# Kernel tuning notes

Hardware: AMD Instinct MI355X
Metric: run time of the kernel (lower is better)

## Reference

```python
import jax, jax.numpy as jnp
import numpy as np

DIM = 768
N_HEAD = 12
HEAD_DIM = 64
INNER = N_HEAD * HEAD_DIM
SCALE = HEAD_DIM ** -0.5


def setup_inputs() -> dict:
    key = jax.random.key(0)
    ks = jax.random.split(key, 12)
    B, Sf, St = 4, 2048, 2048
    from_tensor = jax.random.normal(ks[0], (B, Sf, DIM), dtype=jnp.float32)
    to_tensor = jax.random.normal(ks[1], (B, St, DIM), dtype=jnp.float32)
    attention_mask = jax.random.randint(ks[2], (B, Sf, St), 0, 2, dtype=jnp.int32)
    # Dense layers: kernel ~ RandomNormal (stddev 0.05, keras default), bias zeros
    def kern(k, fan_in, fan_out):
        return 0.05 * jax.random.normal(k, (fan_in, fan_out), dtype=jnp.float32)
    return {
        "from_tensor": from_tensor,
        "to_tensor": to_tensor,
        "attention_mask": attention_mask,
        "Wq": kern(ks[3], DIM, INNER), "bq": jnp.zeros((INNER,), jnp.float32),
        "Wk": kern(ks[4], DIM, INNER), "bk": jnp.zeros((INNER,), jnp.float32),
        "Wv": kern(ks[5], DIM, INNER), "bv": jnp.zeros((INNER,), jnp.float32),
        "Wo": kern(ks[6], INNER, DIM), "bo": jnp.zeros((DIM,), jnp.float32),
    }


def reference(from_tensor, to_tensor, attention_mask, Wq, bq, Wk, bk, Wv, bv, Wo, bo):
    B, Sf, _ = from_tensor.shape
    St = to_tensor.shape[1]
    # projections -> [B, S, n_head, head_dim] -> [B, n_head, S, head_dim]
    def split_heads(x, S):
        return x.reshape(B, S, N_HEAD, HEAD_DIM).transpose(0, 2, 1, 3)
    q = split_heads(from_tensor @ Wq + bq, Sf) * SCALE
    k = split_heads(to_tensor @ Wk + bk, St)
    v = split_heads(to_tensor @ Wv + bv, St)
    # scores [B, H, Sf, St]
    scores = jnp.einsum('bhik,bhjk->bhij', q, k)
    adder = (1.0 - attention_mask.astype(jnp.float32)) * -10000.0
    scores = scores + adder[:, None, :, :]
    probs = jax.nn.softmax(scores, axis=-1)
    out = jnp.einsum('bhij,bhjk->bhik', probs, v)  # [B, H, Sf, Dh]
    out = out.transpose(0, 2, 1, 3).reshape(B, Sf, INNER)
    return out @ Wo + bo
```

## Files before the change

### kernel.cpp

```cpp
#include <hip/hip_runtime.h>
#include <stdint.h>

#define DIM 768
#define NH 12
#define HD 64
#define BSZ 4
#define SEQ 2048
#define MROWS (BSZ*SEQ)

typedef __attribute__((ext_vector_type(8))) short v8s;
typedef __attribute__((ext_vector_type(4))) float v4f;
typedef __attribute__((ext_vector_type(8))) _Float16 v8h;
typedef __attribute__((ext_vector_type(2))) __fp16 v2fp;

__device__ __forceinline__ uint16_t f2bf(float x) {
  union { float f; uint32_t u; } v; v.f = x;
  uint32_t r = v.u + 0x7fffu + ((v.u >> 16) & 1u);
  return (uint16_t)(r >> 16);
}

#if __has_builtin(__builtin_amdgcn_cvt_pk_bf16_f32)
typedef __attribute__((ext_vector_type(2))) __bf16 v2bf;
__device__ __forceinline__ uint32_t pack_bf16(float a, float b) {
  union { v2bf v; uint32_t u; } c;
  c.v = __builtin_amdgcn_cvt_pk_bf16_f32(a, b);
  return c.u;
}
#else
__device__ __forceinline__ uint32_t pack_bf16(float a, float b) {
  return (uint32_t)f2bf(a) | ((uint32_t)f2bf(b) << 16);
}
#endif

__device__ __forceinline__ uint32_t pack_f16(float a, float b) {
#if __has_builtin(__builtin_amdgcn_cvt_pkrtz)
  union { v2fp h; uint32_t u; } c;
  c.h = __builtin_amdgcn_cvt_pkrtz(a, b);
  return c.u;
#else
  union { _Float16 h[2]; uint32_t u; } c;
  c.h[0] = (_Float16)a; c.h[1] = (_Float16)b; return c.u;
#endif
}

__device__ __forceinline__ float fexp2(float x) {
#if __has_builtin(__builtin_amdgcn_exp2f)
  return __builtin_amdgcn_exp2f(x);
#else
  return exp2f(x);
#endif
}

__device__ __forceinline__ int sbfe1(uint32_t w, int off) {
#if __has_builtin(__builtin_amdgcn_sbfe)
  return __builtin_amdgcn_sbfe((int)w, off, 1);
#else
  return ((int)(w << (31 - off))) >> 31;
#endif
}
__device__ __forceinline__ float maskf(float x, int mext) {
  union { float f; int i; } u; u.f = x; u.i &= mext; return u.f;
}

__device__ __forceinline__ void gl16(const void* g, void* l) {
  __builtin_amdgcn_global_load_lds(
      (const __attribute__((address_space(1))) unsigned int*)g,
      (__attribute__((address_space(3))) unsigned int*)l, 16, 0, 0);
}

__global__ void cvt_bf16_kernel(const float* __restrict__ src0, uint16_t* __restrict__ dst0,
                                const float* __restrict__ src1, uint16_t* __restrict__ dst1,
                                int n4) {
  int i = blockIdx.x * blockDim.x + threadIdx.x;
  const float* src = (i < n4) ? src0 : src1;
  uint16_t* dst = (i < n4) ? dst0 : dst1;
  int j = (i < n4) ? i : i - n4;
  float4 v = ((const float4*)src)[j];
  ushort4 o;
  o.x = f2bf(v.x); o.y = f2bf(v.y); o.z = f2bf(v.z); o.w = f2bf(v.w);
  ((ushort4*)dst)[j] = o;
}

__global__ void mask_bits_kernel(const int* __restrict__ src,
                                 unsigned long long* __restrict__ dst, int nwords) {
  int gtid = blockIdx.x * blockDim.x + threadIdx.x;
  int w = gtid >> 6;
  int lane = threadIdx.x & 63;
  if (w >= nwords) return;
  int b  = w >> 16;
  int q  = (w >> 5) & 2047;
  int kt = w & 31;
  int m = src[((size_t)b * SEQ + q) * SEQ + kt * 64 + lane];
  unsigned long long bits = __ballot(m != 0);
  if (lane == 0) dst[((size_t)b * 32 + kt) * SEQ + q] = bits;
}

__global__ void wtrans_kernel(const float* __restrict__ Wq, const float* __restrict__ Wk,
                              const float* __restrict__ Wv, const float* __restrict__ Wo,
                              uint16_t* __restrict__ WT) {
  __shared__ float tile[32][33];
  int z = blockIdx.z;
  const float* src = (z==0) ? Wq : (z==1) ? Wk : (z==2) ? Wv : Wo;
  uint16_t* dst = WT + (size_t)z * DIM * DIM;
  int tx = threadIdx.x, ty = threadIdx.y;
  int x  = blockIdx.x * 32 + tx;
  int y0 = blockIdx.y * 32;
  for (int j = ty; j < 32; j += 8)
    tile[j][tx] = src[(size_t)(y0 + j) * DIM + x];
  __syncthreads();
  int xo = y0 + tx;
  for (int j = ty; j < 32; j += 8)
    dst[(size_t)(blockIdx.x * 32 + j) * DIM + xo] = f2bf(tile[tx][j]);
}

__global__ __launch_bounds__(256) void gemm_t_kernel(
    const uint16_t* __restrict__ Xf, const uint16_t* __restrict__ Xt,
    const uint16_t* __restrict__ WT, const uint16_t* __restrict__ AO,
    const float* __restrict__ bq, const float* __restrict__ bk,
    const float* __restrict__ bo,
    uint16_t* __restrict__ Qw, uint16_t* __restrict__ Kw,
    float* __restrict__ Out, int mode_base)
{
  __shared__ alignas(16) uint16_t As[128 * 32];
  __shared__ alignas(16) uint16_t Bs[128 * 32];
  int mode = mode_base + blockIdx.z;
  const uint16_t* A = (mode == 0) ? Xf : (mode == 3 ? AO : Xt);
  const uint16_t* W = WT + (size_t)mode * DIM * DIM;
  const float* bias = (mode == 0) ? bq : (mode == 1) ? bk : bo;

  int m0 = blockIdx.x * 128, n0 = blockIdx.y * 128;
  int tid = threadIdx.x;
  int wave = tid >> 6, lane = tid & 63, lr = lane & 15, quad = lane >> 4;
  int wm = (wave >> 1) * 64, wn = (wave & 1) * 64;

  int seg = (lane & 3) ^ ((lane >> 3) & 3);
  const uint16_t* agl = A + (size_t)(m0 + wave * 32 + (lane >> 2)) * DIM + seg * 8;
  const uint16_t* bgl = W + (size_t)(n0 + wave * 32 + (lane >> 2)) * DIM + seg * 8;
  int lb = wave * 1024;
  int ck = (lr >> 1) & 3;

  v4f acc[4][4];
  v4f vz = {0.f, 0.f, 0.f, 0.f};
  #pragma unroll
  for (int j = 0; j < 4; j++)
    #pragma unroll
    for (int i = 0; i < 4; i++) acc[j][i] = vz;

  for (int k0 = 0; k0 < DIM; k0 += 32) {
    __syncthreads();
    gl16(agl + k0,            &As[lb]);
    gl16(agl + k0 + 16 * DIM, &As[lb + 512]);
    gl16(bgl + k0,            &Bs[lb]);
    gl16(bgl + k0 + 16 * DIM, &Bs[lb + 512]);
    __syncthreads();
    v8s af[4], bfr[4];
    #pragma unroll
    for (int i = 0; i < 4; i++)
      af[i] = *(const v8s*)&As[(wm + i * 16 + lr) * 32 + ((quad ^ ck) << 3)];
    #pragma unroll
    for (int j = 0; j < 4; j++)
      bfr[j] = *(const v8s*)&Bs[(wn + j * 16 + lr) * 32 + ((quad ^ ck) << 3)];
    #pragma unroll
    for (int j = 0; j < 4; j++)
      #pragma unroll
      for (int i = 0; i < 4; i++)
        acc[j][i] = __builtin_amdgcn_mfma_f32_16x16x32_bf16(bfr[j], af[i], acc[j][i], 0, 0, 0);
  }

  #pragma unroll
  for (int j = 0; j < 4; j++) {
    int nb = n0 + wn + j * 16 + quad * 4;
    float4 bj4 = *(const float4*)&bias[nb];
    #pragma unroll
    for (int i = 0; i < 4; i++) {
      int m = m0 + wm + i * 16 + lr;
      float v0 = acc[j][i][0] + bj4.x;
      float v1 = acc[j][i][1] + bj4.y;
      float v2 = acc[j][i][2] + bj4.z;
      float v3 = acc[j][i][3] + bj4.w;
      if (mode == 3) {
        float4 o = {v0, v1, v2, v3};
        *(float4*)&Out[(size_t)m * DIM + nb] = o;
      } else {
        if (mode == 0) {
          v0 *= 0.18033688f; v1 *= 0.18033688f;
          v2 *= 0.18033688f; v3 *= 0.18033688f;
        }
        int h = nb >> 6, d = nb & 63;
        int b = m >> 11, s = m & 2047;
        int dd = (mode == 1) ? ((((d >> 3) ^ (s & 7)) << 3) + (d & 7)) : d;
        uint2 pk;
        pk.x = pack_bf16(v0, v1);
        pk.y = pack_bf16(v2, v3);
        uint16_t* Dst = (mode == 0) ? Qw : Kw;
        *(uint2*)&Dst[((size_t)(b * NH + h) * SEQ + s) * HD + dd] = pk;
      }
    }
  }
}

__global__ __launch_bounds__(256) void gemm_v_kernel(
    const uint16_t* __restrict__ Xt, const uint16_t* __restrict__ WT,
    const float* __restrict__ bv, uint16_t* __restrict__ Vw)
{
  __shared__ alignas(16) uint16_t As[128 * 32];
  __shared__ alignas(16) uint16_t Bs[128 * 32];
  const uint16_t* A = Xt;
  const uint16_t* W = WT + (size_t)2 * DIM * DIM;

  int m0 = blockIdx.x * 128, n0 = blockIdx.y * 128;
  int tid = threadIdx.x;
  int wave = tid >> 6, lane = tid & 63, lr = lane & 15, quad = lane >> 4;
  int wm = (wave >> 1) * 64, wn = (wave & 1) * 64;

  int seg = (lane & 3) ^ ((lane >> 3) & 3);
  const uint16_t* agl = A + (size_t)(m0 + wave * 32 + (lane >> 2)) * DIM + seg * 8;
  const uint16_t* bgl = W + (size_t)(n0 + wave * 32 + (lane >> 2)) * DIM + seg * 8;
  int lb = wave * 1024;
  int ck = (lr >> 1) & 3;

  v4f acc[4][4];
  v4f vz = {0.f, 0.f, 0.f, 0.f};
  #pragma unroll
  for (int i = 0; i < 4; i++)
    #pragma unroll
    for (int j = 0; j < 4; j++) acc[i][j] = vz;

  for (int k0 = 0; k0 < DIM; k0 += 32) {
    __syncthreads();
    gl16(agl + k0,            &As[lb]);
    gl16(agl + k0 + 16 * DIM, &As[lb + 512]);
    gl16(bgl + k0,            &Bs[lb]);
    gl16(bgl + k0 + 16 * DIM, &Bs[lb + 512]);
    __syncthreads();
    v8s af[4], bfr[4];
    #pragma unroll
    for (int i = 0; i < 4; i++)
      af[i] = *(const v8s*)&As[(wm + i * 16 + lr) * 32 + ((quad ^ ck) << 3)];
    #pragma unroll
    for (int j = 0; j < 4; j++)
      bfr[j] = *(const v8s*)&Bs[(wn + j * 16 + lr) * 32 + ((quad ^ ck) << 3)];
    #pragma unroll
    for (int i = 0; i < 4; i++)
      #pragma unroll
      for (int j = 0; j < 4; j++)
        acc[i][j] = __builtin_amdgcn_mfma_f32_16x16x32_bf16(af[i], bfr[j], acc[i][j], 0, 0, 0);
  }

  float bj[4];
  #pragma unroll
  for (int j = 0; j < 4; j++) bj[j] = bv[n0 + wn + j * 16 + lr];

  #pragma unroll
  for (int i = 0; i < 4; i++) {
    int m = m0 + wm + i * 16 + quad * 4;
    int b = m >> 11, s0 = m & 2047;
    int kk0 = s0 & 63;
    int pos = (kk0 >> 5) * 32 + ((kk0 >> 2) & 3) * 8 + ((kk0 >> 4) & 1) * 4;
    int chunk = pos >> 3, off = pos & 7;
    #pragma unroll
    for (int j = 0; j < 4; j++) {
      int n = n0 + wn + j * 16 + lr;
      int h = n >> 6, d = n & 63;
      uint2 pk;
      pk.x = pack_f16(acc[i][j][0] + bj[j], acc[i][j][1] + bj[j]);
      pk.y = pack_f16(acc[i][j][2] + bj[j], acc[i][j][3] + bj[j]);
      int idx = (s0 & ~63) + ((chunk ^ (d & 7)) << 3) + off;
      *(uint2*)&Vw[((size_t)(b * NH + h) * HD + d) * SEQ + idx] = pk;
    }
  }
}

__device__ __forceinline__ void softmax8(unsigned long long mw, int sh0,
                                         const v4f* s, v8h* pf) {
  uint32_t mlo = (uint32_t)mw, mhi = (uint32_t)(mw >> 32);
  #pragma unroll
  for (int p = 0; p < 2; p++) {
    float ps[8];
    #pragma unroll
    for (int half = 0; half < 2; half++) {
      int nt = p * 2 + half;
      uint32_t w = (nt < 2) ? mlo : mhi;
      int base = sh0 + ((nt & 1) << 4);
      #pragma unroll
      for (int r = 0; r < 4; r++) {
        float e = fexp2(s[nt][r] - 8.0f);
        ps[half * 4 + r] = maskf(e, sbfe1(w, base + r));
      }
    }
    union { uint4 u; v8h h; } cc;
    cc.u.x = pack_f16(ps[0], ps[1]);
    cc.u.y = pack_f16(ps[2], ps[3]);
    cc.u.z = pack_f16(ps[4], ps[5]);
    cc.u.w = pack_f16(ps[6], ps[7]);
    pf[p] = cc.h;
  }
}

__global__ __launch_bounds__(128, 3) void flash_kernel(
    const uint16_t* __restrict__ Qg, const uint16_t* __restrict__ Kg,
    const uint16_t* __restrict__ Vg, const unsigned long long* __restrict__ Mb,
    uint16_t* __restrict__ AO)
{
  __shared__ alignas(16) uint16_t Ks[64 * 64];
  __shared__ alignas(16) uint16_t Vs[64 * 64];

  int tid = threadIdx.x, wave = tid >> 6, lane = tid & 63, lr = lane & 15, quad = lane >> 4;
  int bh = blockIdx.y;
  int b = bh / NH, h = bh - b * NH;
  int q0 = blockIdx.x * 64;
  const uint16_t* Qp = Qg + (size_t)bh * SEQ * HD;
  const uint16_t* Kp = Kg + (size_t)bh * SEQ * HD;
  const uint16_t* Vp = Vg + (size_t)bh * HD * SEQ;
  int qg0 = q0 + wave * 32 + lr;
  int qg1 = qg0 + 16;
  const unsigned long long* Mp0 = Mb + (size_t)b * 32 * SEQ + qg0;
  const unsigned long long* Mp1 = Mp0 + 16;

  int swk = lr & 7, sh0 = quad * 4;

  v8s qf0a = *(const v8s*)&Qp[(size_t)qg0 * HD + quad * 8];
  v8s qf0b = *(const v8s*)&Qp[(size_t)qg0 * HD + 32 + quad * 8];
  v8s qf1a = *(const v8s*)&Qp[(size_t)qg1 * HD + quad * 8];
  v8s qf1b = *(const v8s*)&Qp[(size_t)qg1 * HD + 32 + quad * 8];

  const uint16_t* kgl = Kp + ((size_t)(wave * 32 + (lane >> 3)) * HD + (lane & 7) * 8);
  const uint16_t* vgl = Vp + ((size_t)(wave * 32 + (lane >> 3)) * SEQ + (lane & 7) * 8);
  int lb = wave * 2048;

  int koff[4][2], voff[4][2];
  #pragma unroll
  for (int nt = 0; nt < 4; nt++) {
    int rowb = (nt * 16 + lr) << 6;
    koff[nt][0] = rowb + ((quad ^ swk) << 3);
    koff[nt][1] = rowb + (((quad + 4) ^ swk) << 3);
    voff[nt][0] = rowb + ((quad ^ swk) << 3);
    voff[nt][1] = rowb + (((quad + 4) ^ swk) << 3);
  }

  v8h ones;
  #pragma unroll
  for (int e = 0; e < 8; e++) ones[e] = (_Float16)1.0f;

  v4f acc0[4], acc1[4], accs0, accs1;
  v4f vz = {0.f, 0.f, 0.f, 0.f};
  #pragma unroll
  for (int dt = 0; dt < 4; dt++) { acc0[dt] = vz; acc1[dt] = vz; }
  accs0 = vz; accs1 = vz;

  unsigned long long nm0 = Mp0[0], nm1 = Mp1[0];

  for (int k0 = 0; k0 < SEQ; k0 += 64) {
    __syncthreads();
    #pragma unroll
    for (int c = 0; c < 4; c++) {
      gl16(kgl + ((size_t)k0 + c * 8) * HD, &Ks[lb + c * 512]);
      gl16(vgl + k0 + (size_t)c * 8 * SEQ, &Vs[lb + c * 512]);
    }
    unsigned long long mw0 = nm0, mw1 = nm1;
    size_t nidx = (size_t)((k0 >> 6) + 1) * SEQ;
    nm0 = Mp0[nidx]; nm1 = Mp1[nidx];
    __syncthreads();

    v4f s0[4], s1[4];
    #pragma unroll
    for (int nt = 0; nt < 4; nt++) {
      v8s kf0 = *(const v8s*)&Ks[koff[nt][0]];
      v8s kf1 = *(const v8s*)&Ks[koff[nt][1]];
      v4f z = vz;
      z = __builtin_amdgcn_mfma_f32_16x16x32_bf16(kf0, qf0a, z, 0, 0, 0);
      z = __builtin_amdgcn_mfma_f32_16x16x32_bf16(kf1, qf0b, z, 0, 0, 0);
      s0[nt] = z;
      z = vz;
      z = __builtin_amdgcn_mfma_f32_16x16x32_bf16(kf0, qf1a, z, 0, 0, 0);
      z = __builtin_amdgcn_mfma_f32_16x16x32_bf16(kf1, qf1b, z, 0, 0, 0);
      s1[nt] = z;
    }

    v8h pf0[2], pf1[2];
    softmax8(mw0, sh0, s0, pf0);
    softmax8(mw1, sh0, s1, pf1);

    #pragma unroll
    for (int dt = 0; dt < 4; dt++) {
      #pragma unroll
      for (int p = 0; p < 2; p++) {
        v8h vv = *(const v8h*)&Vs[voff[dt][p]];
        acc0[dt] = __builtin_amdgcn_mfma_f32_16x16x32_f16(vv, pf0[p], acc0[dt], 0, 0, 0);
        acc1[dt] = __builtin_amdgcn_mfma_f32_16x16x32_f16(vv, pf1[p], acc1[dt], 0, 0, 0);
      }
    }
    #pragma unroll
    for (int p = 0; p < 2; p++) {
      accs0 = __builtin_amdgcn_mfma_f32_16x16x32_f16(ones, pf0[p], accs0, 0, 0, 0);
      accs1 = __builtin_amdgcn_mfma_f32_16x16x32_f16(ones, pf1[p], accs1, 0, 0, 0);
    }
  }

  float ri0 = 1.0f / accs0[0];
  float ri1 = 1.0f / accs1[0];

  #pragma unroll
  for (int dt = 0; dt < 4; dt++) {
    uint2 pk;
    pk.x = pack_bf16(acc0[dt][0] * ri0, acc0[dt][1] * ri0);
    pk.y = pack_bf16(acc0[dt][2] * ri0, acc0[dt][3] * ri0);
    *(uint2*)&AO[(size_t)(b * SEQ + qg0) * DIM + h * HD + dt * 16 + sh0] = pk;
    pk.x = pack_bf16(acc1[dt][0] * ri1, acc1[dt][1] * ri1);
    pk.y = pack_bf16(acc1[dt][2] * ri1, acc1[dt][3] * ri1);
    *(uint2*)&AO[(size_t)(b * SEQ + qg1) * DIM + h * HD + dt * 16 + sh0] = pk;
  }
}

extern "C" void kernel_launch(void* const* d_in, const int* in_sizes, int n_in,
                              void* d_out, int out_size, void* d_ws, size_t ws_size,
                              hipStream_t stream) {
  const float* from_t = (const float*)d_in[0];
  const float* to_t   = (const float*)d_in[1];
  const int*   maski  = (const int*)d_in[2];
  const float* Wq = (const float*)d_in[3];  const float* bq = (const float*)d_in[4];
  const float* Wk = (const float*)d_in[5];  const float* bk = (const float*)d_in[6];
  const float* Wv = (const float*)d_in[7];  const float* bv = (const float*)d_in[8];
  const float* Wo = (const float*)d_in[9];  const float* bo = (const float*)d_in[10];

  char* ws = (char*)d_ws;
  size_t off = 0;
  uint16_t* Xf = (uint16_t*)(ws + off); off += (size_t)MROWS * DIM * 2;
  uint16_t* Xt = (uint16_t*)(ws + off); off += (size_t)MROWS * DIM * 2;
  uint16_t* WT = (uint16_t*)(ws + off); off += (size_t)4 * DIM * DIM * 2;
  unsigned long long* Mbits = (unsigned long long*)(ws + off);
  off += (size_t)(BSZ * 32 + 1) * SEQ * 8;
  uint16_t* Qw = (uint16_t*)(ws + off); off += (size_t)MROWS * DIM * 2;
  uint16_t* Kw = (uint16_t*)(ws + off); off += (size_t)MROWS * DIM * 2;
  uint16_t* Vw = (uint16_t*)(ws + off); off += (size_t)MROWS * DIM * 2;
  uint16_t* AO = (uint16_t*)(ws + off); off += (size_t)MROWS * DIM * 2;
  float* Out = (float*)d_out;

  int nx4 = MROWS * DIM / 4;
  cvt_bf16_kernel<<<2 * nx4 / 256, 256, 0, stream>>>(from_t, Xf, to_t, Xt, nx4);
  int nwords = BSZ * 32 * SEQ;
  mask_bits_kernel<<<nwords * 64 / 256, 256, 0, stream>>>(maski, Mbits, nwords);
  wtrans_kernel<<<dim3(24, 24, 4), dim3(32, 8), 0, stream>>>(Wq, Wk, Wv, Wo, WT);

  gemm_t_kernel<<<dim3(64, 6, 2), 256, 0, stream>>>(Xf, Xt, WT, AO, bq, bk, bo,
                                                    Qw, Kw, Out, 0);
  gemm_v_kernel<<<dim3(64, 6), 256, 0, stream>>>(Xt, WT, bv, Vw);
  flash_kernel<<<dim3(SEQ / 64, BSZ * NH), 128, 0, stream>>>(Qw, Kw, Vw, Mbits, AO);
  gemm_t_kernel<<<dim3(64, 6, 1), 256, 0, stream>>>(Xf, Xt, WT, AO, bq, bk, bo,
                                                    Qw, Kw, Out, 3);
}
```

Measured before the change: 333.9 us.

## Merge QKV/O GEMMs into single-wave double-buffered DMA GEMM kernel

Replaces the two 256-thread 128x128 GEMM kernels with one 64-thread kernel computing 64x64 tiles, covering Q, K, V (and the output projection) in one launch. Global-to-LDS loads are double-buffered and overlapped with MFMA through manual vmcnt waits instead of block barriers. This removes one launch and the __syncthreads stalls, in exchange for less data reuse per tile and more blocks. The flash kernel also reuses the K offsets for V reads, dropping a duplicate register array.

```diff
diff --git a/kernel.cpp b/kernel.cpp
--- a/kernel.cpp
+++ b/kernel.cpp
@@ -113,160 +113,131 @@
     dst[(size_t)(blockIdx.x * 32 + j) * DIM + xo] = f2bf(tile[tx][j]);
 }
 
-__global__ __launch_bounds__(256) void gemm_t_kernel(
+__global__ __launch_bounds__(64) void gemm_dma_kernel(
     const uint16_t* __restrict__ Xf, const uint16_t* __restrict__ Xt,
     const uint16_t* __restrict__ WT, const uint16_t* __restrict__ AO,
     const float* __restrict__ bq, const float* __restrict__ bk,
-    const float* __restrict__ bo,
-    uint16_t* __restrict__ Qw, uint16_t* __restrict__ Kw,
+    const float* __restrict__ bv, const float* __restrict__ bo,
+    uint16_t* __restrict__ Qw, uint16_t* __restrict__ Kw, uint16_t* __restrict__ Vw,
     float* __restrict__ Out, int mode_base)
 {
-  __shared__ alignas(16) uint16_t As[128 * 32];
-  __shared__ alignas(16) uint16_t Bs[128 * 32];
-  int mode = mode_base + blockIdx.z;
+  __shared__ alignas(16) uint16_t As[2][2048];
+  __shared__ alignas(16) uint16_t Bs[2][2048];
+  int mode = mode_base + blockIdx.y;
   const uint16_t* A = (mode == 0) ? Xf : (mode == 3 ? AO : Xt);
   const uint16_t* W = WT + (size_t)mode * DIM * DIM;
-  const float* bias = (mode == 0) ? bq : (mode == 1) ? bk : bo;
-
-  int m0 = blockIdx.x * 128, n0 = blockIdx.y * 128;
-  int tid = threadIdx.x;
-  int wave = tid >> 6, lane = tid & 63, lr = lane & 15, quad = lane >> 4;
-  int wm = (wave >> 1) * 64, wn = (wave & 1) * 64;
-
+
+  int bx = blockIdx.x;
+  int mt = bx & 127, ntile = bx >> 7;
+  int m0 = mt << 6, n0 = ntile << 6;
+  int lane = threadIdx.x;
+  int lr = lane & 15, quad = lane >> 4;
   int seg = (lane & 3) ^ ((lane >> 3) & 3);
-  const uint16_t* agl = A + (size_t)(m0 + wave * 32 + (lane >> 2)) * DIM + seg * 8;
-  const uint16_t* bgl = W + (size_t)(n0 + wave * 32 + (lane >> 2)) * DIM + seg * 8;
-  int lb = wave * 1024;
+  const uint16_t* agl = A + (size_t)(m0 + (lane >> 2)) * DIM + seg * 8;
+  const uint16_t* bgl = W + (size_t)(n0 + (lane >> 2)) * DIM + seg * 8;
   int ck = (lr >> 1) & 3;
 
   v4f acc[4][4];
   v4f vz = {0.f, 0.f, 0.f, 0.f};
   #pragma unroll
-  for (int j = 0; j < 4; j++)
-    #pragma unroll
-    for (int i = 0; i < 4; i++) acc[j][i] = vz;
-
-  for (int k0 = 0; k0 < DIM; k0 += 32) {
-    __syncthreads();
-    gl16(agl + k0,            &As[lb]);
-    gl16(agl + k0 + 16 * DIM, &As[lb + 512]);
-    gl16(bgl + k0,            &Bs[lb]);
-    gl16(bgl + k0 + 16 * DIM, &Bs[lb + 512]);
-    __syncthreads();
-    v8s af[4], bfr[4];
-    #pragma unroll
-    for (int i = 0; i < 4; i++)
-      af[i] = *(const v8s*)&As[(wm + i * 16 + lr) * 32 + ((quad ^ ck) << 3)];
-    #pragma unroll
-    for (int j = 0; j < 4; j++)
-      bfr[j] = *(const v8s*)&Bs[(wn + j * 16 + lr) * 32 + ((quad ^ ck) << 3)];
-    #pragma unroll
-    for (int j = 0; j < 4; j++)
-      #pragma unroll
-      for (int i = 0; i < 4; i++)
-        acc[j][i] = __builtin_amdgcn_mfma_f32_16x16x32_bf16(bfr[j], af[i], acc[j][i], 0, 0, 0);
-  }
-
-  #pragma unroll
-  for (int j = 0; j < 4; j++) {
-    int nb = n0 + wn + j * 16 + quad * 4;
-    float4 bj4 = *(const float4*)&bias[nb];
+  for (int i = 0; i < 4; i++)
+    #pragma unroll
+    for (int j = 0; j < 4; j++) acc[i][j] = vz;
+
+  #pragma unroll
+  for (int c = 0; c < 4; c++) {
+    gl16(agl + c * 16 * DIM, &As[0][c * 512]);
+    gl16(bgl + c * 16 * DIM, &Bs[0][c * 512]);
+  }
+
+  #pragma unroll 2
+  for (int i = 0; i < 24; i++) {
+    int buf = i & 1;
+    if (i < 23) {
+      int k1 = (i + 1) * 32;
+      asm volatile("s_waitcnt lgkmcnt(0)" ::: "memory");
+      #pragma unroll
+      for (int c = 0; c < 4; c++) {
+        gl16(agl + k1 + c * 16 * DIM, &As[buf ^ 1][c * 512]);
+        gl16(bgl + k1 + c * 16 * DIM, &Bs[buf ^ 1][c * 512]);
+      }
+      asm volatile("s_waitcnt vmcnt(8)" ::: "memory");
+    } else {
+      asm volatile("s_waitcnt vmcnt(0)" ::: "memory");
+    }
+    v8s af[4], bf[4];
+    #pragma unroll
+    for (int t = 0; t < 4; t++) {
+      af[t] = *(const v8s*)&As[buf][(t * 16 + lr) * 32 + ((quad ^ ck) << 3)];
+      bf[t] = *(const v8s*)&Bs[buf][(t * 16 + lr) * 32 + ((quad ^ ck) << 3)];
+    }
+    if (mode == 2) {
+      #pragma unroll
+      for (int ti = 0; ti < 4; ti++)
+        #pragma unroll
+        for (int tj = 0; tj < 4; tj++)
+          acc[ti][tj] = __builtin_amdgcn_mfma_f32_16x16x32_bf16(af[ti], bf[tj], acc[ti][tj], 0, 0, 0);
+    } else {
+      #pragma unroll
+      for (int tj = 0; tj < 4; tj++)
+        #pragma unroll
+        for (int ti = 0; ti < 4; ti++)
+          acc[tj][ti] = __builtin_amdgcn_mfma_f32_16x16x32_bf16(bf[tj], af[ti], acc[tj][ti], 0, 0, 0);
+    }
+  }
+
+  if (mode == 2) {
+    float bj[4];
+    #pragma unroll
+    for (int j = 0; j < 4; j++) bj[j] = bv[n0 + j * 16 + lr];
     #pragma unroll
     for (int i = 0; i < 4; i++) {
-      int m = m0 + wm + i * 16 + lr;
-      float v0 = acc[j][i][0] + bj4.x;
-      float v1 = acc[j][i][1] + bj4.y;
-      float v2 = acc[j][i][2] + bj4.z;
-      float v3 = acc[j][i][3] + bj4.w;
-      if (mode == 3) {
-        float4 o = {v0, v1, v2, v3};
-        *(float4*)&Out[(size_t)m * DIM + nb] = o;
-      } else {
-        if (mode == 0) {
-          v0 *= 0.18033688f; v1 *= 0.18033688f;
-          v2 *= 0.18033688f; v3 *= 0.18033688f;
+      int m = m0 + i * 16 + quad * 4;
+      int b = m >> 11, s0 = m & 2047;
+      int kk0 = s0 & 63;
+      int pos = (kk0 >> 5) * 32 + ((kk0 >> 2) & 3) * 8 + ((kk0 >> 4) & 1) * 4;
+      int chunk = pos >> 3, off = pos & 7;
+      #pragma unroll
+      for (int j = 0; j < 4; j++) {
+        int d = j * 16 + lr;
+        uint2 pk;
+        pk.x = pack_f16(acc[i][j][0] + bj[j], acc[i][j][1] + bj[j]);
+        pk.y = pack_f16(acc[i][j][2] + bj[j], acc[i][j][3] + bj[j]);
+        int idx = (s0 & ~63) + ((chunk ^ (d & 7)) << 3) + off;
+        *(uint2*)&Vw[((size_t)(b * NH + ntile) * HD + d) * SEQ + idx] = pk;
+      }
+    }
+  } else {
+    const float* bias = (mode == 0) ? bq : (mode == 1) ? bk : bo;
+    #pragma unroll
+    for (int j = 0; j < 4; j++) {
+      int nb = n0 + j * 16 + quad * 4;
+      float4 bj4 = *(const float4*)&bias[nb];
+      #pragma unroll
+      for (int i = 0; i < 4; i++) {
+        int m = m0 + i * 16 + lr;
+        float v0 = acc[j][i][0] + bj4.x;
+        float v1 = acc[j][i][1] + bj4.y;
+        float v2 = acc[j][i][2] + bj4.z;
+        float v3 = acc[j][i][3] + bj4.w;
+        if (mode == 3) {
+          float4 o = {v0, v1, v2, v3};
+          *(float4*)&Out[(size_t)m * DIM + nb] = o;
+        } else {
+          if (mode == 0) {
+            v0 *= 0.18033688f; v1 *= 0.18033688f;
+            v2 *= 0.18033688f; v3 *= 0.18033688f;
+          }
+          int d0 = nb & 63;
+          int b = m >> 11, s = m & 2047;
+          int dd = (mode == 1) ? ((((d0 >> 3) ^ (s & 7)) << 3) + (d0 & 7)) : d0;
+          uint2 pk;
+          pk.x = pack_bf16(v0, v1);
+          pk.y = pack_bf16(v2, v3);
+          uint16_t* Dst = (mode == 0) ? Qw : Kw;
+          *(uint2*)&Dst[((size_t)(b * NH + ntile) * SEQ + s) * HD + dd] = pk;
         }
-        int h = nb >> 6, d = nb & 63;
-        int b = m >> 11, s = m & 2047;
-        int dd = (mode == 1) ? ((((d >> 3) ^ (s & 7)) << 3) + (d & 7)) : d;
-        uint2 pk;
-        pk.x = pack_bf16(v0, v1);
-        pk.y = pack_bf16(v2, v3);
-        uint16_t* Dst = (mode == 0) ? Qw : Kw;
-        *(uint2*)&Dst[((size_t)(b * NH + h) * SEQ + s) * HD + dd] = pk;
       }
-    }
-  }
-}
-
-__global__ __launch_bounds__(256) void gemm_v_kernel(
-    const uint16_t* __restrict__ Xt, const uint16_t* __restrict__ WT,
-    const float* __restrict__ bv, uint16_t* __restrict__ Vw)
-{
-  __shared__ alignas(16) uint16_t As[128 * 32];
-  __shared__ alignas(16) uint16_t Bs[128 * 32];
-  const uint16_t* A = Xt;
-  const uint16_t* W = WT + (size_t)2 * DIM * DIM;
-
-  int m0 = blockIdx.x * 128, n0 = blockIdx.y * 128;
-  int tid = threadIdx.x;
-  int wave = tid >> 6, lane = tid & 63, lr = lane & 15, quad = lane >> 4;
-  int wm = (wave >> 1) * 64, wn = (wave & 1) * 64;
-
-  int seg = (lane & 3) ^ ((lane >> 3) & 3);
-  const uint16_t* agl = A + (size_t)(m0 + wave * 32 + (lane >> 2)) * DIM + seg * 8;
-  const uint16_t* bgl = W + (size_t)(n0 + wave * 32 + (lane >> 2)) * DIM + seg * 8;
-  int lb = wave * 1024;
-  int ck = (lr >> 1) & 3;
-
-  v4f acc[4][4];
-  v4f vz = {0.f, 0.f, 0.f, 0.f};
-  #pragma unroll
-  for (int i = 0; i < 4; i++)
-    #pragma unroll
-    for (int j = 0; j < 4; j++) acc[i][j] = vz;
-
-  for (int k0 = 0; k0 < DIM; k0 += 32) {
-    __syncthreads();
-    gl16(agl + k0,            &As[lb]);
-    gl16(agl + k0 + 16 * DIM, &As[lb + 512]);
-    gl16(bgl + k0,            &Bs[lb]);
-    gl16(bgl + k0 + 16 * DIM, &Bs[lb + 512]);
-    __syncthreads();
-    v8s af[4], bfr[4];
-    #pragma unroll
-    for (int i = 0; i < 4; i++)
-      af[i] = *(const v8s*)&As[(wm + i * 16 + lr) * 32 + ((quad ^ ck) << 3)];
-    #pragma unroll
-    for (int j = 0; j < 4; j++)
-      bfr[j] = *(const v8s*)&Bs[(wn + j * 16 + lr) * 32 + ((quad ^ ck) << 3)];
-    #pragma unroll
-    for (int i = 0; i < 4; i++)
-      #pragma unroll
-      for (int j = 0; j < 4; j++)
-        acc[i][j] = __builtin_amdgcn_mfma_f32_16x16x32_bf16(af[i], bfr[j], acc[i][j], 0, 0, 0);
-  }
-
-  float bj[4];
-  #pragma unroll
-  for (int j = 0; j < 4; j++) bj[j] = bv[n0 + wn + j * 16 + lr];
-
-  #pragma unroll
-  for (int i = 0; i < 4; i++) {
-    int m = m0 + wm + i * 16 + quad * 4;
-    int b = m >> 11, s0 = m & 2047;
-    int kk0 = s0 & 63;
-    int pos = (kk0 >> 5) * 32 + ((kk0 >> 2) & 3) * 8 + ((kk0 >> 4) & 1) * 4;
-    int chunk = pos >> 3, off = pos & 7;
-    #pragma unroll
-    for (int j = 0; j < 4; j++) {
-      int n = n0 + wn + j * 16 + lr;
-      int h = n >> 6, d = n & 63;
-      uint2 pk;
-      pk.x = pack_f16(acc[i][j][0] + bj[j], acc[i][j][1] + bj[j]);
-      pk.y = pack_f16(acc[i][j][2] + bj[j], acc[i][j][3] + bj[j]);
-      int idx = (s0 & ~63) + ((chunk ^ (d & 7)) << 3) + off;
-      *(uint2*)&Vw[((size_t)(b * NH + h) * HD + d) * SEQ + idx] = pk;
     }
   }
 }
@@ -328,14 +299,12 @@
   const uint16_t* vgl = Vp + ((size_t)(wave * 32 + (lane >> 3)) * SEQ + (lane & 7) * 8);
   int lb = wave * 2048;
 
-  int koff[4][2], voff[4][2];
+  int koff[4][2];
   #pragma unroll
   for (int nt = 0; nt < 4; nt++) {
     int rowb = (nt * 16 + lr) << 6;
     koff[nt][0] = rowb + ((quad ^ swk) << 3);
     koff[nt][1] = rowb + (((quad + 4) ^ swk) << 3);
-    voff[nt][0] = rowb + ((quad ^ swk) << 3);
-    voff[nt][1] = rowb + (((quad + 4) ^ swk) << 3);
   }
 
   v8h ones;
@@ -385,7 +354,7 @@
     for (int dt = 0; dt < 4; dt++) {
       #pragma unroll
       for (int p = 0; p < 2; p++) {
-        v8h vv = *(const v8h*)&Vs[voff[dt][p]];
+        v8h vv = *(const v8h*)&Vs[koff[dt][p]];
         acc0[dt] = __builtin_amdgcn_mfma_f32_16x16x32_f16(vv, pf0[p], acc0[dt], 0, 0, 0);
         acc1[dt] = __builtin_amdgcn_mfma_f32_16x16x32_f16(vv, pf1[p], acc1[dt], 0, 0, 0);
       }
@@ -442,10 +411,9 @@
   mask_bits_kernel<<<nwords * 64 / 256, 256, 0, stream>>>(maski, Mbits, nwords);
   wtrans_kernel<<<dim3(24, 24, 4), dim3(32, 8), 0, stream>>>(Wq, Wk, Wv, Wo, WT);
 
-  gemm_t_kernel<<<dim3(64, 6, 2), 256, 0, stream>>>(Xf, Xt, WT, AO, bq, bk, bo,
-                                                    Qw, Kw, Out, 0);
-  gemm_v_kernel<<<dim3(64, 6), 256, 0, stream>>>(Xt, WT, bv, Vw);
+  gemm_dma_kernel<<<dim3(1536, 3), 64, 0, stream>>>(Xf, Xt, WT, AO, bq, bk, bv, bo,
+                                                    Qw, Kw, Vw, Out, 0);
   flash_kernel<<<dim3(SEQ / 64, BSZ * NH), 128, 0, stream>>>(Qw, Kw, Vw, Mbits, AO);
-  gemm_t_kernel<<<dim3(64, 6, 1), 256, 0, stream>>>(Xf, Xt, WT, AO, bq, bk, bo,
-                                                    Qw, Kw, Out, 3);
-}
+  gemm_dma_kernel<<<dim3(1536, 1), 64, 0, stream>>>(Xf, Xt, WT, AO, bq, bk, bv, bo,
+                                                    Qw, Kw, Vw, Out, 3);
+}
```

New measurement: 349.2 us. 4.6% more time.
